# Performance work log

Measured on AMD Instinct MI355X. Metric: run time of the kernel, lower is better.

Reference implementation:

```python
import jax, jax.numpy as jnp
import numpy as np

NUM_C = 1000
DIM_S = 128
SIZE_M = 64
B = 64
L = 512


def setup_inputs() -> dict:
    key = jax.random.key(0)
    ks = jax.random.split(key, 16)
    d = DIM_S
    inp = {
        "q": jax.random.randint(ks[0], (B, L), 0, NUM_C),
        "r": jax.random.randint(ks[1], (B, L), 0, 2),
        # embeddings
        "Ek": jax.random.normal(ks[2], (NUM_C, d), jnp.float32),
        "Ev": jax.random.normal(ks[3], (2 * NUM_C, d), jnp.float32),
        # memory key / initial value memory (kaiming-normal-ish)
        "Mk": jax.random.normal(ks[4], (SIZE_M, d), jnp.float32) * np.sqrt(2.0 / d),
        "Mv0": jax.random.normal(ks[5], (SIZE_M, d), jnp.float32) * np.sqrt(2.0 / d),
        # erase / add layers (d -> d)
        "We": jax.random.normal(ks[6], (d, d), jnp.float32) / np.sqrt(d),
        "be": jnp.zeros((d,), jnp.float32),
        "Wa": jax.random.normal(ks[7], (d, d), jnp.float32) / np.sqrt(d),
        "ba": jnp.zeros((d,), jnp.float32),
        # f layer (2d -> d)
        "Wf": jax.random.normal(ks[8], (2 * d, d), jnp.float32) / np.sqrt(2 * d),
        "bf": jnp.zeros((d,), jnp.float32),
        # p layer (d -> 1)
        "Wp": jax.random.normal(ks[9], (d, 1), jnp.float32) / np.sqrt(d),
        "bp": jnp.zeros((1,), jnp.float32),
    }
    return inp


def reference(q, r, Ek, Ev, Mk, Mv0, We, be, Wa, ba, Wf, bf, Wp, bp):
    # q, r: [B, L] int
    x = q + NUM_C * r
    k = Ek[q]            # [B, L, D]  (k_original; no extra features when use_ed=use_mp=0)
    v = Ev[x]            # [B, L, D]

    # correlation weights over memory slots
    w = jax.nn.softmax(jnp.einsum("bld,md->blm", k, Mk), axis=-1)  # [B, L, M]

    e = jax.nn.sigmoid(v @ We + be)  # [B, L, D] erase
    a = jnp.tanh(v @ Wa + ba)        # [B, L, D] add

    def step(Mvt, inputs):
        wt, et, at = inputs            # [B,M], [B,D], [B,D]
        # read from memory BEFORE the update (matches Mv[:, :-1] in torch)
        read = jnp.einsum("bm,bmd->bd", wt, Mvt)
        Mvt_new = Mvt * (1.0 - wt[:, :, None] * et[:, None, :]) + wt[:, :, None] * at[:, None, :]
        return Mvt_new, read

    Mv_init = jnp.broadcast_to(Mv0[None], (q.shape[0], SIZE_M, DIM_S))
    xs = (jnp.swapaxes(w, 0, 1), jnp.swapaxes(e, 0, 1), jnp.swapaxes(a, 0, 1))
    _, reads = jax.lax.scan(step, Mv_init, xs)      # reads: [L, B, D]
    read_content = jnp.swapaxes(reads, 0, 1)        # [B, L, D]

    f = jnp.tanh(jnp.concatenate([read_content, k], axis=-1) @ Wf + bf)  # [B, L, D]
    # dropout in eval mode -> identity
    p = jax.nn.sigmoid(f @ Wp + bp)[..., 0]         # [B, L]
    return p
```

## Files before the change

kernel.cpp:

```cpp
#include <hip/hip_runtime.h>
#include <hip/hip_bf16.h>

#define NUM_C 1000
#define DIM   128
#define MM    64
#define BB    64
#define LL    512
#define NROWS (BB * LL)

typedef unsigned short u16;
typedef unsigned int   u32;
typedef short bfrag __attribute__((ext_vector_type(8)));
typedef float f32x4 __attribute__((ext_vector_type(4)));

__device__ __forceinline__ float sigmoidf_fast(float x) { return 1.f / (1.f + __expf(-x)); }
__device__ __forceinline__ float tanhf_fast(float x) { return 1.f - 2.f / (__expf(2.f * x) + 1.f); }

__device__ __forceinline__ u16 f2bf(float x) {
    u32 u = __float_as_uint(x);
    return (u16)((u + 0x7FFFu + ((u >> 16) & 1u)) >> 16);
}
__device__ __forceinline__ float bf2f(u16 h) { return __uint_as_float(((u32)h) << 16); }

__device__ __forceinline__ float quad_swap1(float x) {
    return __int_as_float(__builtin_amdgcn_mov_dpp(__float_as_int(x), 0xB1, 0xF, 0xF, true));
}
__device__ __forceinline__ float quad_swap2(float x) {
    return __int_as_float(__builtin_amdgcn_mov_dpp(__float_as_int(x), 0x4E, 0xF, 0xF, true));
}
__device__ __forceinline__ float swz_xor4(float x) {
    return __int_as_float(__builtin_amdgcn_ds_swizzle(__float_as_int(x), 0x101F));
}

__device__ __forceinline__ void ld16(const void* g, void* l) {
    __builtin_amdgcn_global_load_lds(
        (const __attribute__((address_space(1))) unsigned int*)g,
        (__attribute__((address_space(3))) unsigned int*)l, 16, 0, 0);
}

__global__ __launch_bounds__(256) void kP(const float* __restrict__ We,
                                          const float* __restrict__ Wa,
                                          const float* __restrict__ Wf,
                                          const float* __restrict__ Mk,
                                          u16* weT_hi, u16* weT_lo,
                                          u16* waT_hi, u16* waT_lo,
                                          u16* wfT_hi, u16* wfT_lo,
                                          u16* mkT_hi, u16* mkT_lo) {
    int idx = blockIdx.x * 256 + threadIdx.x;
    if (idx < 128 * 128) {
        int n = idx >> 7, k = idx & 127;
        float we = We[k * DIM + n];
        u16 h = f2bf(we);
        weT_hi[idx] = h; weT_lo[idx] = f2bf(we - bf2f(h));
        float wa = Wa[k * DIM + n];
        u16 h2 = f2bf(wa);
        waT_hi[idx] = h2; waT_lo[idx] = f2bf(wa - bf2f(h2));
    }
    if (idx < 64 * 128) {
        float mk = Mk[idx];
        u16 h = f2bf(mk);
        mkT_hi[idx] = h; mkT_lo[idx] = f2bf(mk - bf2f(h));
    }
    {
        int n = idx >> 8, k = idx & 255;
        float wf = Wf[k * DIM + n];
        u16 h = f2bf(wf);
        wfT_hi[idx] = h; wfT_lo[idx] = f2bf(wf - bf2f(h));
    }
}

__device__ __forceinline__ void split8(const float* src, bfrag& h, bfrag& l) {
    float4 f0 = *reinterpret_cast<const float4*>(src);
    float4 f1 = *reinterpret_cast<const float4*>(src + 4);
    float xs[8] = {f0.x, f0.y, f0.z, f0.w, f1.x, f1.y, f1.z, f1.w};
    #pragma unroll
    for (int j = 0; j < 8; ++j) {
        u16 hb = f2bf(xs[j]);
        h[j] = (short)hb;
        l[j] = (short)f2bf(xs[j] - bf2f(hb));
    }
}

__global__ __launch_bounds__(256) void kA(const int* __restrict__ q,
                                          const float* __restrict__ Ek,
                                          const u16* __restrict__ mkT_hi,
                                          const u16* __restrict__ mkT_lo,
                                          float* __restrict__ w_out) {
    __shared__ __align__(16) u16 khi[4][16][136];
    __shared__ __align__(16) u16 klo[4][16][136];
    __shared__ float slab[4][64];
    const int tid = threadIdx.x;
    const int base = blockIdx.x * 64;

    {
        const int row_l = tid >> 2;
        const int rts = row_l >> 4, ms = row_l & 15;
        const int d0 = (tid & 3) * 32;
        const float* src = Ek + (size_t)q[base + row_l] * DIM + d0;
        #pragma unroll
        for (int c8 = 0; c8 < 4; ++c8) {
            bfrag h, l;
            split8(src + c8 * 8, h, l);
            *reinterpret_cast<bfrag*>(&khi[rts][ms][d0 + c8 * 8]) = h;
            *reinterpret_cast<bfrag*>(&klo[rts][ms][d0 + c8 * 8]) = l;
        }
    }
    __syncthreads();

    const int lane = tid & 63;
    const int wv = tid >> 6;
    const int nloc = lane & 15;
    const int quad = lane >> 4;
    const int n = wv * 16 + nloc;

    bfrag Bh[4], Bl[4];
    #pragma unroll
    for (int kc = 0; kc < 4; ++kc) {
        const int ko = kc * 32 + quad * 8;
        Bh[kc] = *reinterpret_cast<const bfrag*>(mkT_hi + n * DIM + ko);
        Bl[kc] = *reinterpret_cast<const bfrag*>(mkT_lo + n * DIM + ko);
    }

    f32x4 acc[4];
    #pragma unroll
    for (int t = 0; t < 4; ++t) acc[t] = 0.f;

    #pragma unroll
    for (int rt = 0; rt < 4; ++rt) {
        #pragma unroll
        for (int kc = 0; kc < 4; ++kc) {
            const int ko = kc * 32 + quad * 8;
            bfrag Ah = *reinterpret_cast<const bfrag*>(&khi[rt][nloc][ko]);
            bfrag Al = *reinterpret_cast<const bfrag*>(&klo[rt][nloc][ko]);
            acc[rt] = __builtin_amdgcn_mfma_f32_16x16x32_bf16(Ah, Bh[kc], acc[rt], 0, 0, 0);
            acc[rt] = __builtin_amdgcn_mfma_f32_16x16x32_bf16(Ah, Bl[kc], acc[rt], 0, 0, 0);
            acc[rt] = __builtin_amdgcn_mfma_f32_16x16x32_bf16(Al, Bh[kc], acc[rt], 0, 0, 0);
        }
    }

    float ex[4][4];
    #pragma unroll
    for (int rt = 0; rt < 4; ++rt) {
        #pragma unroll
        for (int rg = 0; rg < 4; ++rg) {
            float e = __expf(acc[rt][rg]);
            ex[rt][rg] = e;
            float s = e;
            s += __shfl_xor(s, 1);
            s += __shfl_xor(s, 2);
            s += __shfl_xor(s, 4);
            s += __shfl_xor(s, 8);
            if (nloc == 0) slab[wv][rt * 16 + quad * 4 + rg] = s;
        }
    }
    __syncthreads();

    #pragma unroll
    for (int rt = 0; rt < 4; ++rt) {
        #pragma unroll
        for (int rg = 0; rg < 4; ++rg) {
            const int row = rt * 16 + quad * 4 + rg;
            float tot = slab[0][row] + slab[1][row] + slab[2][row] + slab[3][row];
            w_out[(size_t)(base + row) * MM + n] = ex[rt][rg] / tot;
        }
    }
}

__global__ __launch_bounds__(256) void kB(const int* __restrict__ q,
                                          const int* __restrict__ r,
                                          const float* __restrict__ Ev,
                                          const u16* __restrict__ weT_hi, const u16* __restrict__ weT_lo,
                                          const u16* __restrict__ waT_hi, const u16* __restrict__ waT_lo,
                                          const float* __restrict__ be, const float* __restrict__ ba,
                                          float2* __restrict__ ea_out) {
    __shared__ __align__(16) u16 vhi[4][16][136];
    __shared__ __align__(16) u16 vlo[4][16][136];
    const int tid = threadIdx.x;
    const int base = blockIdx.x * 64;

    {
        const int row_l = tid >> 2;
        const int rts = row_l >> 4, ms = row_l & 15;
        const int d0 = (tid & 3) * 32;
        const int row = base + row_l;
        const int x = q[row] + NUM_C * r[row];
        const float* src = Ev + (size_t)x * DIM + d0;
        #pragma unroll
        for (int c8 = 0; c8 < 4; ++c8) {
            bfrag h, l;
            split8(src + c8 * 8, h, l);
            *reinterpret_cast<bfrag*>(&vhi[rts][ms][d0 + c8 * 8]) = h;
            *reinterpret_cast<bfrag*>(&vlo[rts][ms][d0 + c8 * 8]) = l;
        }
    }
    __syncthreads();

    const int lane = tid & 63;
    const int wv = tid >> 6;
    const int nloc = lane & 15;
    const int quad = lane >> 4;

    #pragma unroll
    for (int dt = 0; dt < 2; ++dt) {
        const int n = (wv * 2 + dt) * 16 + nloc;
        bfrag Beh[4], Bel[4], Bah[4], Bal[4];
        #pragma unroll
        for (int kc = 0; kc < 4; ++kc) {
            const int ko = kc * 32 + quad * 8;
            Beh[kc] = *reinterpret_cast<const bfrag*>(weT_hi + n * DIM + ko);
            Bel[kc] = *reinterpret_cast<const bfrag*>(weT_lo + n * DIM + ko);
            Bah[kc] = *reinterpret_cast<const bfrag*>(waT_hi + n * DIM + ko);
            Bal[kc] = *reinterpret_cast<const bfrag*>(waT_lo + n * DIM + ko);
        }
        f32x4 acc_e[4], acc_a[4];
        #pragma unroll
        for (int t = 0; t < 4; ++t) { acc_e[t] = 0.f; acc_a[t] = 0.f; }

        #pragma unroll
        for (int rt = 0; rt < 4; ++rt) {
            #pragma unroll
            for (int kc = 0; kc < 4; ++kc) {
                const int ko = kc * 32 + quad * 8;
                bfrag Ah = *reinterpret_cast<const bfrag*>(&vhi[rt][nloc][ko]);
                bfrag Al = *reinterpret_cast<const bfrag*>(&vlo[rt][nloc][ko]);
                acc_e[rt] = __builtin_amdgcn_mfma_f32_16x16x32_bf16(Ah, Beh[kc], acc_e[rt], 0, 0, 0);
                acc_a[rt] = __builtin_amdgcn_mfma_f32_16x16x32_bf16(Ah, Bah[kc], acc_a[rt], 0, 0, 0);
                acc_e[rt] = __builtin_amdgcn_mfma_f32_16x16x32_bf16(Ah, Bel[kc], acc_e[rt], 0, 0, 0);
                acc_a[rt] = __builtin_amdgcn_mfma_f32_16x16x32_bf16(Ah, Bal[kc], acc_a[rt], 0, 0, 0);
                acc_e[rt] = __builtin_amdgcn_mfma_f32_16x16x32_bf16(Al, Beh[kc], acc_e[rt], 0, 0, 0);
                acc_a[rt] = __builtin_amdgcn_mfma_f32_16x16x32_bf16(Al, Bah[kc], acc_a[rt], 0, 0, 0);
            }
        }
        const float bev = be[n], bav = ba[n];
        #pragma unroll
        for (int rt = 0; rt < 4; ++rt) {
            #pragma unroll
            for (int rg = 0; rg < 4; ++rg) {
                const int row = base + rt * 16 + quad * 4 + rg;
                float2 ea;
                ea.x = sigmoidf_fast(acc_e[rt][rg] + bev);
                ea.y = tanhf_fast(acc_a[rt][rg] + bav);
                ea_out[(size_t)row * DIM + n] = ea;
            }
        }
    }
}

__device__ __forceinline__ void scan32(const float* wb, const float2* eab,
                                       int m0, int dl, int p, int t0,
                                       float (&Mv)[8], float* rp) {
    #pragma unroll
    for (int u = 0; u < 32; ++u) {
        float4 w0 = *reinterpret_cast<const float4*>(wb + u * 64 + m0);
        float4 w1 = *reinterpret_cast<const float4*>(wb + u * 64 + m0 + 4);
        float2 ea = eab[u * 32 + dl];
        float wv[8] = {w0.x, w0.y, w0.z, w0.w, w1.x, w1.y, w1.z, w1.w};
        float e_c = ea.x, a_c = ea.y;
        float p0 = 0.f, p1 = 0.f;
        #pragma unroll
        for (int j = 0; j < 4; ++j) {
            float old = Mv[j];
            p0 = fmaf(wv[j], old, p0);
            Mv[j] = fmaf(wv[j], fmaf(-old, e_c, a_c), old);
        }
        #pragma unroll
        for (int j = 4; j < 8; ++j) {
            float old = Mv[j];
            p1 = fmaf(wv[j], old, p1);
            Mv[j] = fmaf(wv[j], fmaf(-old, e_c, a_c), old);
        }
        float part = p0 + p1;
        part += swz_xor4(part);
        part += quad_swap2(part);
        part += quad_swap1(part);
        if (p == 0) rp[(size_t)(t0 + u) * DIM] = part;
    }
}

__global__ __launch_bounds__(256) void kC(const float* __restrict__ Mv0,
                                          const float* __restrict__ w_in,
                                          const float2* __restrict__ ea_in,
                                          float* __restrict__ read_buf) {
    __shared__ __align__(16) float  wlds[2][32][64];
    __shared__ __align__(16) float2 ealds[2][32][32];
    const int tid = threadIdx.x;
    const int lane = tid & 63;
    const int wvid = tid >> 6;
    const int p = tid & 7;
    const int dl = tid >> 3;
    const int ds = blockIdx.x, b = blockIdx.y;
    const int d = ds * 32 + dl;
    const int m0 = p * 8;

    const char* wsrc  = (const char*)(w_in + (size_t)b * LL * MM);
    const char* easrc = (const char*)(ea_in + (size_t)b * LL * DIM + ds * 32);
    float* rp = read_buf + (size_t)b * LL * DIM + d;

    auto dma = [&](int c, int bufi) {
        const char* wt = wsrc + (size_t)c * 8192;
        char* wl = (char*)&wlds[bufi][0][0];
        char* el = (char*)&ealds[bufi][0][0];
        #pragma unroll
        for (int i = 0; i < 2; ++i) {
            const int off = wvid * 2048 + i * 1024 + lane * 16;
            ld16(wt + off, wl + off);
            const int tl = off >> 8, wi = off & 255;
            ld16(easrc + (size_t)(c * 32 + tl) * (DIM * 8) + wi, el + off);
        }
    };

    dma(0, 0);

    float Mv[8];
    #pragma unroll
    for (int j = 0; j < 8; ++j)
        Mv[j] = Mv0[(m0 + j) * DIM + d];

    int buf = 0;
    for (int c = 0; c < LL / 32; ++c) {
        __builtin_amdgcn_s_waitcnt(0x0F70);
        __syncthreads();
        if (c + 1 < LL / 32) dma(c + 1, buf ^ 1);
        scan32(&wlds[buf][0][0], &ealds[buf][0][0], m0, dl, p, c * 32, Mv, rp);
        buf ^= 1;
    }
}

__global__ __launch_bounds__(256) void kD(const int* __restrict__ q,
                                          const float* __restrict__ Ek,
                                          const u16* __restrict__ wfT_hi, const u16* __restrict__ wfT_lo,
                                          const float* __restrict__ bfv,
                                          const float* __restrict__ Wp, const float* __restrict__ bp,
                                          const float* __restrict__ read_buf,
                                          float* __restrict__ out) {
    __shared__ __align__(16) u16 xhi[4][16][264];
    __shared__ __align__(16) u16 xlo[4][16][264];
    __shared__ float sred[64][4];
    const int tid = threadIdx.x;
    const int base = blockIdx.x * 64;
    const int row_l = tid >> 2;
    const int rts = row_l >> 4, ms = row_l & 15;
    const int d0 = (tid & 3) * 32;
    const int row = base + row_l;

    {
        const float* src = read_buf + (size_t)row * DIM + d0;
        #pragma unroll
        for (int c8 = 0; c8 < 4; ++c8) {
            bfrag h, l;
            split8(src + c8 * 8, h, l);
            *reinterpret_cast<bfrag*>(&xhi[rts][ms][d0 + c8 * 8]) = h;
            *reinterpret_cast<bfrag*>(&xlo[rts][ms][d0 + c8 * 8]) = l;
        }
    }
    {
        const float* src = Ek + (size_t)q[row] * DIM + d0;
        #pragma unroll
        for (int c8 = 0; c8 < 4; ++c8) {
            bfrag h, l;
            split8(src + c8 * 8, h, l);
            *reinterpret_cast<bfrag*>(&xhi[rts][ms][128 + d0 + c8 * 8]) = h;
            *reinterpret_cast<bfrag*>(&xlo[rts][ms][128 + d0 + c8 * 8]) = l;
        }
    }
    __syncthreads();

    const int lane = tid & 63;
    const int wv = tid >> 6;
    const int nloc = lane & 15;
    const int quad = lane >> 4;
    float* fbuf = reinterpret_cast<float*>(&xhi[0][0][0]);

    f32x4 acc[2][4];
    #pragma unroll
    for (int dt = 0; dt < 2; ++dt)
        #pragma unroll
        for (int t = 0; t < 4; ++t) acc[dt][t] = 0.f;

    #pragma unroll
    for (int dt = 0; dt < 2; ++dt) {
        const int n = (wv * 2 + dt) * 16 + nloc;
        bfrag Bh[8], Bl[8];
        #pragma unroll
        for (int kc = 0; kc < 8; ++kc) {
            const int ko = kc * 32 + quad * 8;
            Bh[kc] = *reinterpret_cast<const bfrag*>(wfT_hi + n * 256 + ko);
            Bl[kc] = *reinterpret_cast<const bfrag*>(wfT_lo + n * 256 + ko);
        }
        #pragma unroll
        for (int rt = 0; rt < 4; ++rt) {
            #pragma unroll
            for (int kc = 0; kc < 8; ++kc) {
                const int ko = kc * 32 + quad * 8;
                bfrag Ah = *reinterpret_cast<const bfrag*>(&xhi[rt][nloc][ko]);
                bfrag Al = *reinterpret_cast<const bfrag*>(&xlo[rt][nloc][ko]);
                acc[dt][rt] = __builtin_amdgcn_mfma_f32_16x16x32_bf16(Ah, Bh[kc], acc[dt][rt], 0, 0, 0);
                acc[dt][rt] = __builtin_amdgcn_mfma_f32_16x16x32_bf16(Ah, Bl[kc], acc[dt][rt], 0, 0, 0);
                acc[dt][rt] = __builtin_amdgcn_mfma_f32_16x16x32_bf16(Al, Bh[kc], acc[dt][rt], 0, 0, 0);
            }
        }
    }
    __syncthreads();

    #pragma unroll
    for (int dt = 0; dt < 2; ++dt) {
        const int n = (wv * 2 + dt) * 16 + nloc;
        const float bfn = bfv[n], wpn = Wp[n];
        #pragma unroll
        for (int rt = 0; rt < 4; ++rt)
            #pragma unroll
            for (int rg = 0; rg < 4; ++rg)
                fbuf[(rt * 16 + quad * 4 + rg) * 132 + n] = tanhf_fast(acc[dt][rt][rg] + bfn) * wpn;
    }
    __syncthreads();

    {
        float s = 0.f;
        const int c = tid & 3;
        #pragma unroll
        for (int k = 0; k < 32; ++k) s += fbuf[row_l * 132 + c * 32 + k];
        sred[row_l][c] = s;
    }
    __syncthreads();
    if (tid < 64)
        out[base + tid] = sigmoidf_fast(sred[tid][0] + sred[tid][1] + sred[tid][2] + sred[tid][3] + bp[0]);
}

extern "C" void kernel_launch(void* const* d_in, const int* in_sizes, int n_in,
                              void* d_out, int out_size, void* d_ws, size_t ws_size,
                              hipStream_t stream) {
    const int*   q   = (const int*)d_in[0];
    const int*   r   = (const int*)d_in[1];
    const float* Ek  = (const float*)d_in[2];
    const float* Ev  = (const float*)d_in[3];
    const float* Mk  = (const float*)d_in[4];
    const float* Mv0 = (const float*)d_in[5];
    const float* We  = (const float*)d_in[6];
    const float* be  = (const float*)d_in[7];
    const float* Wa  = (const float*)d_in[8];
    const float* ba  = (const float*)d_in[9];
    const float* Wf  = (const float*)d_in[10];
    const float* bfv = (const float*)d_in[11];
    const float* Wp  = (const float*)d_in[12];
    const float* bp  = (const float*)d_in[13];
    float* out = (float*)d_out;

    float*  ws     = (float*)d_ws;
    float*  w_buf  = ws;
    float2* ea_buf = (float2*)(w_buf + (size_t)NROWS * MM);
    float*  rd_buf = (float*)(ea_buf + (size_t)NROWS * DIM);

    size_t prep_off = (ws_size - (size_t)294912) & ~(size_t)255;
    u16* weT_hi = (u16*)((char*)d_ws + prep_off);
    u16* weT_lo = weT_hi + 16384;
    u16* waT_hi = weT_lo + 16384;
    u16* waT_lo = waT_hi + 16384;
    u16* wfT_hi = waT_lo + 16384;
    u16* wfT_lo = wfT_hi + 32768;
    u16* mkT_hi = wfT_lo + 32768;
    u16* mkT_lo = mkT_hi + 8192;

    kP<<<dim3(128), 256, 0, stream>>>(We, Wa, Wf, Mk, weT_hi, weT_lo, waT_hi, waT_lo,
                                      wfT_hi, wfT_lo, mkT_hi, mkT_lo);
    kA<<<dim3(NROWS / 64), 256, 0, stream>>>(q, Ek, mkT_hi, mkT_lo, w_buf);
    kB<<<dim3(NROWS / 64), 256, 0, stream>>>(q, r, Ev, weT_hi, weT_lo, waT_hi, waT_lo,
                                             be, ba, ea_buf);
    kC<<<dim3(4, BB), 256, 0, stream>>>(Mv0, w_buf, ea_buf, rd_buf);
    kD<<<dim3(NROWS / 64), 256, 0, stream>>>(q, Ek, wfT_hi, wfT_lo, bfv, Wp, bp, rd_buf, out);
}
```

Measured before the change: 200.3 us.

## Defer final read reduction to consumer kernel and move scan barrier after compute

After: 192.5 us. 1.04x faster.

```diff
diff --git a/kernel.cpp b/kernel.cpp
--- a/kernel.cpp
+++ b/kernel.cpp
@@ -27,9 +27,6 @@
 }
 __device__ __forceinline__ float quad_swap2(float x) {
     return __int_as_float(__builtin_amdgcn_mov_dpp(__float_as_int(x), 0x4E, 0xF, 0xF, true));
-}
-__device__ __forceinline__ float swz_xor4(float x) {
-    return __int_as_float(__builtin_amdgcn_ds_swizzle(__float_as_int(x), 0x101F));
 }
 
 __device__ __forceinline__ void ld16(const void* g, void* l) {
@@ -248,7 +245,7 @@
 
 __device__ __forceinline__ void scan32(const float* wb, const float2* eab,
                                        int m0, int dl, int p, int t0,
-                                       float (&Mv)[8], float* rp) {
+                                       float (&Mv)[8], float* rp2) {
     #pragma unroll
     for (int u = 0; u < 32; ++u) {
         float4 w0 = *reinterpret_cast<const float4*>(wb + u * 64 + m0);
@@ -270,17 +267,17 @@
             Mv[j] = fmaf(wv[j], fmaf(-old, e_c, a_c), old);
         }
         float part = p0 + p1;
-        part += swz_xor4(part);
+        part += quad_swap1(part);
         part += quad_swap2(part);
-        part += quad_swap1(part);
-        if (p == 0) rp[(size_t)(t0 + u) * DIM] = part;
+        if ((p & 3) == 0)
+            rp2[(size_t)(t0 + u) * (2 * DIM)] = part;
     }
 }
 
 __global__ __launch_bounds__(256) void kC(const float* __restrict__ Mv0,
                                           const float* __restrict__ w_in,
                                           const float2* __restrict__ ea_in,
-                                          float* __restrict__ read_buf) {
+                                          float* __restrict__ rd2) {
     __shared__ __align__(16) float  wlds[2][32][64];
     __shared__ __align__(16) float2 ealds[2][32][32];
     const int tid = threadIdx.x;
@@ -294,7 +291,7 @@
 
     const char* wsrc  = (const char*)(w_in + (size_t)b * LL * MM);
     const char* easrc = (const char*)(ea_in + (size_t)b * LL * DIM + ds * 32);
-    float* rp = read_buf + (size_t)b * LL * DIM + d;
+    float* rp2 = rd2 + (size_t)b * LL * (2 * DIM) + (size_t)d * 2 + (p >> 2);
 
     auto dma = [&](int c, int bufi) {
         const char* wt = wsrc + (size_t)c * 8192;
@@ -316,13 +313,18 @@
     for (int j = 0; j < 8; ++j)
         Mv[j] = Mv0[(m0 + j) * DIM + d];
 
+    __builtin_amdgcn_s_waitcnt(0x0F70);
+    __syncthreads();
+
     int buf = 0;
     for (int c = 0; c < LL / 32; ++c) {
-        __builtin_amdgcn_s_waitcnt(0x0F70);
-        __syncthreads();
         if (c + 1 < LL / 32) dma(c + 1, buf ^ 1);
-        scan32(&wlds[buf][0][0], &ealds[buf][0][0], m0, dl, p, c * 32, Mv, rp);
-        buf ^= 1;
+        scan32(&wlds[buf][0][0], &ealds[buf][0][0], m0, dl, p, c * 32, Mv, rp2);
+        if (c + 1 < LL / 32) {
+            __builtin_amdgcn_s_waitcnt(0x8F70);
+            __syncthreads();
+            buf ^= 1;
+        }
     }
 }
 
@@ -331,7 +333,7 @@
                                           const u16* __restrict__ wfT_hi, const u16* __restrict__ wfT_lo,
                                           const float* __restrict__ bfv,
                                           const float* __restrict__ Wp, const float* __restrict__ bp,
-                                          const float* __restrict__ read_buf,
+                                          const float* __restrict__ rd2,
                                           float* __restrict__ out) {
     __shared__ __align__(16) u16 xhi[4][16][264];
     __shared__ __align__(16) u16 xlo[4][16][264];
@@ -344,11 +346,22 @@
     const int row = base + row_l;
 
     {
-        const float* src = read_buf + (size_t)row * DIM + d0;
+        const float2* src2 = reinterpret_cast<const float2*>(rd2 + (size_t)row * (2 * DIM)) + d0;
         #pragma unroll
         for (int c8 = 0; c8 < 4; ++c8) {
+            float xs[8];
+            #pragma unroll
+            for (int j = 0; j < 8; ++j) {
+                float2 v = src2[c8 * 8 + j];
+                xs[j] = v.x + v.y;
+            }
             bfrag h, l;
-            split8(src + c8 * 8, h, l);
+            #pragma unroll
+            for (int j = 0; j < 8; ++j) {
+                u16 hb = f2bf(xs[j]);
+                h[j] = (short)hb;
+                l[j] = (short)f2bf(xs[j] - bf2f(hb));
+            }
             *reinterpret_cast<bfrag*>(&xhi[rts][ms][d0 + c8 * 8]) = h;
             *reinterpret_cast<bfrag*>(&xlo[rts][ms][d0 + c8 * 8]) = l;
         }
@@ -448,7 +461,7 @@
     float*  ws     = (float*)d_ws;
     float*  w_buf  = ws;
     float2* ea_buf = (float2*)(w_buf + (size_t)NROWS * MM);
-    float*  rd_buf = (float*)(ea_buf + (size_t)NROWS * DIM);
+    float*  rd2    = (float*)(ea_buf + (size_t)NROWS * DIM);
 
     size_t prep_off = (ws_size - (size_t)294912) & ~(size_t)255;
     u16* weT_hi = (u16*)((char*)d_ws + prep_off);
@@ -465,6 +478,6 @@
     kA<<<dim3(NROWS / 64), 256, 0, stream>>>(q, Ek, mkT_hi, mkT_lo, w_buf);
     kB<<<dim3(NROWS / 64), 256, 0, stream>>>(q, r, Ev, weT_hi, weT_lo, waT_hi, waT_lo,
                                              be, ba, ea_buf);
-    kC<<<dim3(4, BB), 256, 0, stream>>>(Mv0, w_buf, ea_buf, rd_buf);
-    kD<<<dim3(NROWS / 64), 256, 0, stream>>>(q, Ek, wfT_hi, wfT_lo, bfv, Wp, bp, rd_buf, out);
-}
+    kC<<<dim3(4, BB), 256, 0, stream>>>(Mv0, w_buf, ea_buf, rd2);
+    kD<<<dim3(NROWS / 64), 256, 0, stream>>>(q, Ek, wfT_hi, wfT_lo, bfv, Wp, bp, rd2, out);
+}
```
